# Optimization experiments

Hardware: AMD Instinct MI355X
Metric: run time of the kernel (lower is better)

Reference implementation:

```python
import jax, jax.numpy as jnp
import numpy as np

DIM = 128
NUM_HEADS = 4
SPLIT_SIZE = 8
HEAD_DIM = DIM // NUM_HEADS
SCALE = HEAD_DIM ** -0.5


def setup_inputs() -> dict:
    key = jax.random.key(0)
    qkv = jax.random.normal(key, (3, 8, 4096, DIM), dtype=jnp.float32)
    return {"qkv": qkv, "H": 64, "W": 64}


def _to_windows(x, H, W, H_sp, W_sp):
    # x: [B, L, C] -> [B*nW, num_heads, H_sp*W_sp, head_dim]
    B, L, C = x.shape
    x = x.reshape(B, H // H_sp, H_sp, W // W_sp, W_sp, C)
    x = x.transpose(0, 1, 3, 2, 4, 5).reshape(-1, H_sp * W_sp, NUM_HEADS, C // NUM_HEADS)
    return x.transpose(0, 2, 1, 3)


def reference(qkv, H, W):
    # idx=0 branch: vertical strips, H_sp = H (full height), W_sp = split_size
    H_sp, W_sp = H, SPLIT_SIZE
    B, L, C = qkv.shape[1], qkv.shape[2], qkv.shape[3]
    q = _to_windows(qkv[0], H, W, H_sp, W_sp) * SCALE
    k = _to_windows(qkv[1], H, W, H_sp, W_sp)
    v = _to_windows(qkv[2], H, W, H_sp, W_sp)
    # [nW, h, S, S] with S = H_sp*W_sp
    attn = jax.nn.softmax(jnp.einsum('whqd,whkd->whqk', q, k), axis=-1)
    x = jnp.einsum('whqk,whkd->whqd', attn, v)
    # merge heads: [nW, S, C]
    x = x.transpose(0, 2, 1, 3).reshape(-1, H_sp * W_sp, C)
    # windows2img: [B, H*W, C]
    x = x.reshape(B, H // H_sp, W // W_sp, H_sp, W_sp, C)
    x = x.transpose(0, 1, 3, 2, 4, 5).reshape(B, H * W, C)
    return x
```

## Files before the change

### kernel.cpp

```cpp
#include <hip/hip_runtime.h>


typedef __attribute__((ext_vector_type(8))) short bf16x8;
typedef __attribute__((ext_vector_type(4))) float f32x4;

#define MFMA16(a, b, c) __builtin_amdgcn_mfma_f32_16x16x32_bf16(a, b, c, 0, 0, 0)
#define KP 40
#define PP 36

__device__ __forceinline__ short f2b(float f) {
    union { float f; unsigned int i; } v; v.f = f;
    unsigned int r = v.i + 0x7fffu + ((v.i >> 16) & 1u);
    return (short)(r >> 16);
}

__global__ __launch_bounds__(256, 2)
void lepe_attn_r6(const float* __restrict__ qkv, float* __restrict__ out)
{
    __shared__ short Ks[256 * KP];
    __shared__ short Vs[256 * KP];
    __shared__ float Pf[4 * 16 * PP];

    const int tid  = threadIdx.x;
    const int wave = tid >> 6;
    const int lane = tid & 63;
    const int col  = lane & 15;
    const int quad = lane >> 4;

    const int blk  = blockIdx.x;
    const int pair = blk >> 2;
    const int qsp  = blk & 3;
    const int wi   = pair >> 2;
    const int hd   = pair & 3;
    const int b    = wi >> 3;
    const int wb   = wi & 7;
    const int chead = hd * 32;

    const size_t baseQ = (size_t)b * 524288;
    const size_t baseK = baseQ + 8u * 524288;
    const size_t baseV = baseQ + 16u * 524288;

    const int q0 = qsp * 128 + wave * 32;
    const float QS   = 0.17677669529663687f * 1.4426950408889634f;
    const float MAXB = 32.0f;
    bf16x8 qf[2];
#pragma unroll
    for (int t = 0; t < 2; ++t) {
        int q  = q0 + t * 16 + col;
        int lq = (q >> 3) * 64 + wb * 8 + (q & 7);
        const float* qp = qkv + baseQ + (size_t)lq * 128 + chead + quad * 8;
        f32x4 qa = *(const f32x4*)qp;
        f32x4 qb = *(const f32x4*)(qp + 4);
        bf16x8 qs;
#pragma unroll
        for (int j = 0; j < 4; ++j) {
            qs[j]     = f2b(qa[j] * QS);
            qs[j + 4] = f2b(qb[j] * QS);
        }
        qf[t] = qs;
    }

    f32x4 o[2][2];
    float lsum[2][4];
#pragma unroll
    for (int t = 0; t < 2; ++t) {
        o[t][0] = (f32x4)0.0f; o[t][1] = (f32x4)0.0f;
#pragma unroll
        for (int r = 0; r < 4; ++r) lsum[t][r] = 0.0f;
    }

    float* Pw = Pf + wave * (16 * PP);

    for (int stage = 0; stage < 2; ++stage) {
        if (stage) __syncthreads();
        const int keybase = stage * 256;
#pragma unroll
        for (int i = 0; i < 4; ++i) {
            int chunk = i * 256 + tid;
            int row   = chunk >> 2;
            int part  = chunk & 3;
            int gk    = keybase + row;
            int lk    = (gk >> 3) * 64 + wb * 8 + (gk & 7);
            size_t goff = (size_t)lk * 128 + chead + part * 8;
            f32x4 k0 = *(const f32x4*)(qkv + baseK + goff);
            f32x4 k1 = *(const f32x4*)(qkv + baseK + goff + 4);
            f32x4 v0 = *(const f32x4*)(qkv + baseV + goff);
            f32x4 v1 = *(const f32x4*)(qkv + baseV + goff + 4);
            bf16x8 kv, vv;
#pragma unroll
            for (int j = 0; j < 4; ++j) {
                kv[j] = f2b(k0[j]); kv[j + 4] = f2b(k1[j]);
                vv[j] = f2b(v0[j]); vv[j + 4] = f2b(v1[j]);
            }
            *(bf16x8*)&Ks[row * KP + part * 8] = kv;
            *(bf16x8*)&Vs[row * KP + part * 8] = vv;
        }
        __syncthreads();

        for (int kb = 0; kb < 256; kb += 32) {
            bf16x8 kf0 = *(const bf16x8*)&Ks[(kb + col) * KP + quad * 8];
            bf16x8 kf1 = *(const bf16x8*)&Ks[(kb + col + 16) * KP + quad * 8];
            bf16x8 vf0, vf1;
#pragma unroll
            for (int j = 0; j < 8; ++j) {
                vf0[j] = Vs[(kb + quad * 8 + j) * KP + col];
                vf1[j] = Vs[(kb + quad * 8 + j) * KP + col + 16];
            }

#pragma unroll
            for (int t = 0; t < 2; ++t) {
                f32x4 s0 = MFMA16(qf[t], kf0, (f32x4)0.0f);
                f32x4 s1 = MFMA16(qf[t], kf1, (f32x4)0.0f);
#pragma unroll
                for (int r = 0; r < 4; ++r) {
                    float p0 = __builtin_exp2f(s0[r] - MAXB);
                    float p1 = __builtin_exp2f(s1[r] - MAXB);
                    int row = quad * 4 + r;
                    Pw[row * PP + col]      = p0;
                    Pw[row * PP + col + 16] = p1;
                    lsum[t][r] += p0 + p1;
                }
                asm volatile("" ::: "memory");
                f32x4 pa = *(const f32x4*)&Pw[col * PP + quad * 8];
                f32x4 pb = *(const f32x4*)&Pw[col * PP + quad * 8 + 4];
                bf16x8 pf;
#pragma unroll
                for (int j = 0; j < 4; ++j) {
                    pf[j] = f2b(pa[j]); pf[j + 4] = f2b(pb[j]);
                }
                asm volatile("" ::: "memory");
                o[t][0] = MFMA16(pf, vf0, o[t][0]);
                o[t][1] = MFMA16(pf, vf1, o[t][1]);
            }
        }
    }

    const size_t baseO = (size_t)b * 524288;
#pragma unroll
    for (int t = 0; t < 2; ++t) {
#pragma unroll
        for (int r = 0; r < 4; ++r) {
            float s = lsum[t][r];
            s += __shfl_xor(s, 1);
            s += __shfl_xor(s, 2);
            s += __shfl_xor(s, 4);
            s += __shfl_xor(s, 8);
            float inv = 1.0f / s;
            int q  = q0 + t * 16 + quad * 4 + r;
            int lq = (q >> 3) * 64 + wb * 8 + (q & 7);
            float* orow = out + baseO + (size_t)lq * 128 + chead;
            orow[col]      = o[t][0][r] * inv;
            orow[col + 16] = o[t][1][r] * inv;
        }
    }
}

extern "C" void kernel_launch(void* const* d_in, const int* in_sizes, int n_in,
                              void* d_out, int out_size, void* d_ws, size_t ws_size,
                              hipStream_t stream) {
    const float* qkv = (const float*)d_in[0];
    float* out = (float*)d_out;
    lepe_attn_r6<<<dim3(1024), dim3(256), 0, stream>>>(qkv, out);
}
```

Baseline: 121.2 us.

## Store V transposed and P as packed bf16 with swizzled K in LDS

K is now stored unpadded in LDS with an XOR swizzle, and V is transposed at load time into packed bf16 pairs so each lane reads its V fragment with one vector load instead of sixteen scalar LDS reads. The P tile is written as packed bf16 pairs and rebuilt into MFMA fragments with byte-permute operations, which halves LDS traffic and drops the separate float-to-bf16 conversion pass. The smaller LDS footprint permits launch bounds of 4 blocks per SM, and exp2 now uses the hardware intrinsic. In exchange the V transpose store is a scattered 32-bit write pattern that may cause bank conflicts, and the packing logic adds ALU work.

```diff
diff --git a/kernel.cpp b/kernel.cpp
--- a/kernel.cpp
+++ b/kernel.cpp
@@ -3,23 +3,25 @@
 
 typedef __attribute__((ext_vector_type(8))) short bf16x8;
 typedef __attribute__((ext_vector_type(4))) float f32x4;
+typedef __attribute__((ext_vector_type(4))) int   i32x4;
 
 #define MFMA16(a, b, c) __builtin_amdgcn_mfma_f32_16x16x32_bf16(a, b, c, 0, 0, 0)
-#define KP 40
-#define PP 36
 
-__device__ __forceinline__ short f2b(float f) {
-    union { float f; unsigned int i; } v; v.f = f;
-    unsigned int r = v.i + 0x7fffu + ((v.i >> 16) & 1u);
-    return (short)(r >> 16);
+__device__ __forceinline__ unsigned rne(float f) {
+    union { float f; unsigned u; } v; v.f = f;
+    return v.u + 0x7fffu + ((v.u >> 16) & 1u);
+}
+__device__ __forceinline__ short f2b(float f) { return (short)(rne(f) >> 16); }
+__device__ __forceinline__ unsigned pkhi(unsigned lo, unsigned hi) {
+    return __builtin_amdgcn_perm(hi, lo, 0x07060302u);
 }
 
-__global__ __launch_bounds__(256, 2)
-void lepe_attn_r6(const float* __restrict__ qkv, float* __restrict__ out)
+__global__ __launch_bounds__(256, 4)
+void lepe_attn_r7(const float* __restrict__ qkv, float* __restrict__ out)
 {
-    __shared__ short Ks[256 * KP];
-    __shared__ short Vs[256 * KP];
-    __shared__ float Pf[4 * 16 * PP];
+    __shared__ __align__(16) short    Ks[256 * 32];
+    __shared__ __align__(16) unsigned Vt32[32 * 132];
+    __shared__ __align__(16) unsigned Pb[4 * 16 * 20];
 
     const int tid  = threadIdx.x;
     const int wave = tid >> 6;
@@ -53,10 +55,7 @@
         f32x4 qb = *(const f32x4*)(qp + 4);
         bf16x8 qs;
 #pragma unroll
-        for (int j = 0; j < 4; ++j) {
-            qs[j]     = f2b(qa[j] * QS);
-            qs[j + 4] = f2b(qb[j] * QS);
-        }
+        for (int j = 0; j < 4; ++j) { qs[j] = f2b(qa[j] * QS); qs[j + 4] = f2b(qb[j] * QS); }
         qf[t] = qs;
     }
 
@@ -69,11 +68,12 @@
         for (int r = 0; r < 4; ++r) lsum[t][r] = 0.0f;
     }
 
-    float* Pw = Pf + wave * (16 * PP);
+    unsigned* Pw = Pb + wave * 320;
 
     for (int stage = 0; stage < 2; ++stage) {
         if (stage) __syncthreads();
         const int keybase = stage * 256;
+
 #pragma unroll
         for (int i = 0; i < 4; ++i) {
             int chunk = i * 256 + tid;
@@ -81,31 +81,41 @@
             int part  = chunk & 3;
             int gk    = keybase + row;
             int lk    = (gk >> 3) * 64 + wb * 8 + (gk & 7);
-            size_t goff = (size_t)lk * 128 + chead + part * 8;
-            f32x4 k0 = *(const f32x4*)(qkv + baseK + goff);
-            f32x4 k1 = *(const f32x4*)(qkv + baseK + goff + 4);
-            f32x4 v0 = *(const f32x4*)(qkv + baseV + goff);
-            f32x4 v1 = *(const f32x4*)(qkv + baseV + goff + 4);
-            bf16x8 kv, vv;
+            const float* kp = qkv + baseK + (size_t)lk * 128 + chead + part * 8;
+            f32x4 k0 = *(const f32x4*)kp;
+            f32x4 k1 = *(const f32x4*)(kp + 4);
+            bf16x8 kv;
 #pragma unroll
-            for (int j = 0; j < 4; ++j) {
-                kv[j] = f2b(k0[j]); kv[j + 4] = f2b(k1[j]);
-                vv[j] = f2b(v0[j]); vv[j + 4] = f2b(v1[j]);
-            }
-            *(bf16x8*)&Ks[row * KP + part * 8] = kv;
-            *(bf16x8*)&Vs[row * KP + part * 8] = vv;
+            for (int j = 0; j < 4; ++j) { kv[j] = f2b(k0[j]); kv[j + 4] = f2b(k1[j]); }
+            *(bf16x8*)&Ks[row * 32 + ((part ^ ((row >> 1) & 3)) << 3)] = kv;
+        }
+        {
+            int p    = tid >> 1;
+            int half = tid & 1;
+            int k0g  = keybase + 2 * p;
+            int l0   = (k0g >> 3) * 64 + wb * 8 + (k0g & 7);
+            const float* va = qkv + baseV + (size_t)l0 * 128 + chead + half * 16;
+            const float* vb = va + 128;
+            f32x4 a[4], bb[4];
+#pragma unroll
+            for (int j = 0; j < 4; ++j) { a[j] = *(const f32x4*)(va + 4 * j); bb[j] = *(const f32x4*)(vb + 4 * j); }
+#pragma unroll
+            for (int j = 0; j < 4; ++j)
+#pragma unroll
+                for (int e = 0; e < 4; ++e) {
+                    int dim = half * 16 + j * 4 + e;
+                    Vt32[dim * 132 + p] = pkhi(rne(a[j][e]), rne(bb[j][e]));
+                }
         }
         __syncthreads();
 
         for (int kb = 0; kb < 256; kb += 32) {
-            bf16x8 kf0 = *(const bf16x8*)&Ks[(kb + col) * KP + quad * 8];
-            bf16x8 kf1 = *(const bf16x8*)&Ks[(kb + col + 16) * KP + quad * 8];
-            bf16x8 vf0, vf1;
-#pragma unroll
-            for (int j = 0; j < 8; ++j) {
-                vf0[j] = Vs[(kb + quad * 8 + j) * KP + col];
-                vf1[j] = Vs[(kb + quad * 8 + j) * KP + col + 16];
-            }
+            int r0 = kb + col, r1 = kb + col + 16;
+            bf16x8 kf0 = *(const bf16x8*)&Ks[r0 * 32 + ((quad ^ ((r0 >> 1) & 3)) << 3)];
+            bf16x8 kf1 = *(const bf16x8*)&Ks[r1 * 32 + ((quad ^ ((r1 >> 1) & 3)) << 3)];
+            const short* Vts = (const short*)Vt32;
+            bf16x8 vf0 = *(const bf16x8*)&Vts[col * 264 + kb + quad * 8];
+            bf16x8 vf1 = *(const bf16x8*)&Vts[(col + 16) * 264 + kb + quad * 8];
 
 #pragma unroll
             for (int t = 0; t < 2; ++t) {
@@ -113,21 +123,22 @@
                 f32x4 s1 = MFMA16(qf[t], kf1, (f32x4)0.0f);
 #pragma unroll
                 for (int r = 0; r < 4; ++r) {
-                    float p0 = __builtin_exp2f(s0[r] - MAXB);
-                    float p1 = __builtin_exp2f(s1[r] - MAXB);
-                    int row = quad * 4 + r;
-                    Pw[row * PP + col]      = p0;
-                    Pw[row * PP + col + 16] = p1;
+                    float p0 = __builtin_amdgcn_exp2f(s0[r] - MAXB);
+                    float p1 = __builtin_amdgcn_exp2f(s1[r] - MAXB);
+                    Pw[(quad * 4 + r) * 20 + col] = pkhi(rne(p0), rne(p1));
                     lsum[t][r] += p0 + p1;
                 }
                 asm volatile("" ::: "memory");
-                f32x4 pa = *(const f32x4*)&Pw[col * PP + quad * 8];
-                f32x4 pb = *(const f32x4*)&Pw[col * PP + quad * 8 + 4];
-                bf16x8 pf;
-#pragma unroll
-                for (int j = 0; j < 4; ++j) {
-                    pf[j] = f2b(pa[j]); pf[j + 4] = f2b(pb[j]);
-                }
+                const unsigned* pr = Pw + col * 20 + ((quad & 1) << 3);
+                i32x4 da = *(const i32x4*)pr;
+                i32x4 db = *(const i32x4*)(pr + 4);
+                unsigned sel = (quad < 2) ? 0x05040100u : 0x07060302u;
+                i32x4 fr;
+                fr[0] = (int)__builtin_amdgcn_perm((unsigned)da[1], (unsigned)da[0], sel);
+                fr[1] = (int)__builtin_amdgcn_perm((unsigned)da[3], (unsigned)da[2], sel);
+                fr[2] = (int)__builtin_amdgcn_perm((unsigned)db[1], (unsigned)db[0], sel);
+                fr[3] = (int)__builtin_amdgcn_perm((unsigned)db[3], (unsigned)db[2], sel);
+                bf16x8 pf = __builtin_bit_cast(bf16x8, fr);
                 asm volatile("" ::: "memory");
                 o[t][0] = MFMA16(pf, vf0, o[t][0]);
                 o[t][1] = MFMA16(pf, vf1, o[t][1]);
@@ -160,5 +171,5 @@
                               hipStream_t stream) {
     const float* qkv = (const float*)d_in[0];
     float* out = (float*)d_out;
-    lepe_attn_r6<<<dim3(1024), dim3(256), 0, stream>>>(qkv, out);
+    lepe_attn_r7<<<dim3(1024), dim3(256), 0, stream>>>(qkv, out);
 }
```

Result: faster. 107.9 us (-10.9%).
